# Optimization experiments

Hardware: AMD Instinct MI355X
Metric: run time of the kernel (lower is better)

## Reference

```python
import jax, jax.numpy as jnp
import numpy as np

N, D, DEG, DEPTH, H = 50000, 300, 6, 3, 4
E = N * DEG
DK = D // H


def setup_inputs() -> dict:
    key = jax.random.key(0)
    ks = jax.random.split(key, 14)
    # circulant molecular-like graph: node i <-> i+k (k=1,2,3), edges emitted in
    # reverse pairs (2t, 2t+1) as required by reverse_edge()
    u = np.arange(N)
    src_l, dst_l = [], []
    for k in (1, 2, 3):
        v = (u + k) % N
        src_l.append(np.stack([u, v], 1).reshape(-1))
        dst_l.append(np.stack([v, u], 1).reshape(-1))
    src = np.concatenate(src_l).astype(np.int32)
    dst = np.concatenate(dst_l).astype(np.int32)
    # incoming-edge ids per node (every node has exactly DEG in-edges)
    order = np.argsort(dst, kind='stable')
    nbr_eids = order.reshape(N, DEG).astype(np.int32)
    nbr_mask = np.ones((N, DEG), dtype=bool)
    sd = 1.0 / np.sqrt(D)
    p = lambda i, shape: jax.random.normal(ks[i], shape, jnp.float32) * sd
    return {
        'f': jax.random.normal(ks[0], (N, D), jnp.float32),
        'x': jax.random.normal(ks[1], (E, D), jnp.float32),
        'Wq': p(2, (D, D)), 'bq': jnp.zeros((D,), jnp.float32),
        'Wk': p(3, (D, D)), 'bk': jnp.zeros((D,), jnp.float32),
        'Wv': p(4, (D, D)), 'bv': jnp.zeros((D,), jnp.float32),
        'Wo': p(5, (D, D)), 'bo': jnp.zeros((D,), jnp.float32),
        'W_mp': p(6, (DEPTH - 1, D, D)), 'b_mp': jnp.zeros((DEPTH - 1, D), jnp.float32),
        'W_last': p(7, (3 * D, D)), 'b_last': jnp.zeros((D,), jnp.float32),
        'src': jnp.asarray(src), 'dst': jnp.asarray(dst),
        'nbr_eids': jnp.asarray(nbr_eids), 'nbr_mask': jnp.asarray(nbr_mask),
    }


def reference(f, x, Wq, bq, Wk, bk, Wv, bv, Wo, bo, W_mp, b_mp, W_last, b_last,
              src, dst, nbr_eids, nbr_mask):
    n = f.shape[0]
    e = x.shape[0]
    rev = jnp.arange(e) ^ 1                     # reverse-pair permutation
    has_in = nbr_mask.any(axis=-1)              # [N]
    scale = 1.0 / jnp.sqrt(jnp.float32(DK))
    h = x                                       # edge state 'h' init from 'x'
    f_h = f                                     # node state 'f_h' init from 'f'
    for i in range(DEPTH - 1):
        # ragged mailbox of incoming edge states, padded to DEG
        m = jnp.where(nbr_mask[..., None], h[nbr_eids], 0.0)        # [N,DEG,D]
        q = (f_h @ Wq + bq).reshape(n, H, DK)                        # query = node feat
        k = (m @ Wk + bk).reshape(n, DEG, H, DK)                     # key   = mailbox
        v = ((m + f_h[:, None, :]) @ Wv + bv).reshape(n, DEG, H, DK) # value = mailbox + feat
        scores = jnp.einsum('nhk,ndhk->nhd', q, k) * scale          # [N,H,DEG]
        scores = jnp.where(nbr_mask[:, None, :], scores, -1e9)
        attn = jax.nn.softmax(scores, axis=-1)
        out = jnp.einsum('nhd,ndhk->nhk', attn, v).reshape(n, D) @ Wo + bo
        f_h = jnp.where(has_in[:, None], out, f_h)
        # edge update: m = f_h[src] - rev_h; h = relu(x + Linear_i(m))
        m_e = f_h[src] - h[rev]
        h = jax.nn.relu(x + m_e @ W_mp[i] + b_mp[i])
    # GEANet is undefined in the provided source -> identity pass-through
    mail = jax.ops.segment_sum(h, dst, num_segments=n)              # sum of in-edge states
    f_new = jnp.concatenate([mail, f_h, f], axis=-1) @ W_last + b_last
    f_final = jnp.where(has_in[:, None], f_new, f_h)
    return f_final, h
```

## Files before the change

kernel.cpp:

```cpp
#include <hip/hip_runtime.h>
#include <hip/hip_bf16.h>

typedef unsigned long long ull;
typedef unsigned int u32;
typedef unsigned short u16;
typedef __hip_bfloat16 bf16;
typedef __attribute__((ext_vector_type(8))) short v8s;
typedef __attribute__((ext_vector_type(4))) float v4f;
typedef __attribute__((ext_vector_type(2))) ull v2u;

#define NN 50000
#define DD 300
#define PD 320
#define EE (NN*6)

__device__ __forceinline__ u16 f2bf(float f) {
    u32 u = __float_as_uint(f);
    u32 r = u + 0x7FFFu + ((u >> 16) & 1u);
    return (u16)(r >> 16);
}
__device__ __forceinline__ float bf2f(u16 b) { return __uint_as_float(((u32)b) << 16); }

__device__ __forceinline__ ull sub4bf(ull a, ull b) {
    ull r = 0;
    #pragma unroll
    for (int i = 0; i < 4; ++i) {
        float fa = bf2f((u16)(a >> (16 * i)));
        float fb = bf2f((u16)(b >> (16 * i)));
        r |= ((ull)f2bf(fa - fb)) << (16 * i);
    }
    return r;
}

enum { A_DIR = 0, A_MPG = 1, A_CAT = 2 };
enum { E_BIAS = 0, E_RELUX = 1 };
enum { O_F32 = 1, O_BF16 = 2, O_BOTH = 3 };

template<int AMODE, int EPI, int OUTM, int NW, int NSEG>
__global__ __launch_bounds__(NW*64)
void gemm_mfma(const bf16* __restrict__ A0, const bf16* __restrict__ A1,
               const bf16* __restrict__ A2, const bf16* __restrict__ A3,
               const bf16* __restrict__ A4,
               const int* __restrict__ srcidx, const bf16* __restrict__ BT,
               const float* __restrict__ bias0, const float* __restrict__ bias1,
               const bf16* __restrict__ xepi,
               float* __restrict__ Cf, bf16* __restrict__ Cb0, bf16* __restrict__ Cb1,
               int M)
{
    __shared__ __align__(16) char Als[64 * 640];
    const int tid = threadIdx.x;
    const int wave = tid >> 6, lane = tid & 63;
    const int l15 = lane & 15, l4 = lane >> 4;
    const int wv = (NW == 8) ? (wave & 3) : wave;
    const int half = (NW == 8) ? (wave >> 2) : 0;
    const int rowBase = blockIdx.x * 64;
    const int T = NW * 64;

    v4f acc[4][5];
    const v4f vzero = {0.f, 0.f, 0.f, 0.f};
    #pragma unroll
    for (int mt = 0; mt < 4; ++mt)
        #pragma unroll
        for (int nt = 0; nt < 5; ++nt) acc[mt][nt] = vzero;

    for (int seg = 0; seg < NSEG; ++seg) {
        const bf16* As = (seg == 0) ? A0 : (seg == 1 ? A1 : (seg == 2 ? A2 :
                         (seg == 3 ? A3 : A4)));
        if (seg) __syncthreads();
        #pragma unroll
        for (int s = 0; s < 2560 / T; ++s) {
            int c = tid + T * s;
            int r = c / 40, ch = c - r * 40;
            int grow = rowBase + r;
            int gc = (grow < M) ? grow : 0;
            v2u v;
            if (AMODE == A_MPG) {
                int s0 = srcidx[gc];
                v2u a = *(const v2u*)(A0 + (long)s0 * PD + ch * 8);
                v2u b = *(const v2u*)(A1 + (long)(gc ^ 1) * PD + ch * 8);
                v[0] = sub4bf(a[0], b[0]);
                v[1] = sub4bf(a[1], b[1]);
            } else {
                v = *(const v2u*)(As + (long)gc * PD + ch * 8);
            }
            *(v2u*)(Als + ((c * 16) ^ ((r & 7) << 4))) = v;
        }
        __syncthreads();

        const bf16* BTs = BT + (long)seg * 320 * PD;
        #pragma unroll
        for (int ks = 0; ks < 10; ++ks) {
            v8s af[4];
            #pragma unroll
            for (int mt = 0; mt < 4; ++mt) {
                int rowL = mt * 16 + l15;
                af[mt] = *(const v8s*)(Als +
                    ((rowL * 640 + ks * 64 + l4 * 16) ^ ((rowL & 7) << 4)));
            }
            #pragma unroll
            for (int nt = 0; nt < 5; ++nt) {
                int col = wave * 80 + nt * 16 + l15;
                v8s bfr = *(const v8s*)(BTs + (long)col * PD + ks * 32 + l4 * 8);
                #pragma unroll
                for (int mt = 0; mt < 4; ++mt)
                    acc[mt][nt] = __builtin_amdgcn_mfma_f32_16x16x32_bf16(
                        af[mt], bfr, acc[mt][nt], 0, 0, 0);
            }
        }
        if (seg + 1 < NSEG) __syncthreads();
    }

    const int NOUT = (NW == 8) ? 2 : 1;
    #pragma unroll
    for (int oh = 0; oh < NOUT; ++oh) {
        __syncthreads();
        if (half == oh) {
            const float* bias = oh ? bias1 : bias0;
            #pragma unroll
            for (int nt = 0; nt < 5; ++nt) {
                int col = wv * 80 + nt * 16 + l15;
                float bvv = bias ? bias[col] : 0.f;
                #pragma unroll
                for (int mt = 0; mt < 4; ++mt) {
                    #pragma unroll
                    for (int r = 0; r < 4; ++r) {
                        int rowL = mt * 16 + l4 * 4 + r;
                        *(u16*)(Als + ((rowL * 640 + col * 2) ^ (((rowL >> 2) & 7) << 4)))
                            = f2bf(acc[mt][nt][r] + bvv);
                    }
                }
            }
        }
        __syncthreads();
        {
            bf16* Cb = oh ? Cb1 : Cb0;
            #pragma unroll
            for (int s = 0; s < 2560 / T; ++s) {
                int c = tid + T * s;
                int r = c / 40, ch = c - r * 40;
                int grow = rowBase + r;
                if (grow >= M) continue;
                v2u val = *(const v2u*)(Als + ((c * 16) ^ (((r >> 2) & 7) << 4)));
                if (EPI == E_RELUX) {
                    v2u xv = *(const v2u*)(xepi + (long)grow * PD + ch * 8);
                    #pragma unroll
                    for (int w = 0; w < 2; ++w) {
                        ull rr = 0;
                        #pragma unroll
                        for (int i = 0; i < 4; ++i) {
                            float fv = bf2f((u16)(val[w] >> (16 * i))) +
                                       bf2f((u16)(xv[w] >> (16 * i)));
                            fv = fmaxf(fv, 0.f);
                            rr |= ((ull)f2bf(fv)) << (16 * i);
                        }
                        val[w] = rr;
                    }
                }
                if (OUTM & O_BF16)
                    *(v2u*)(Cb + (long)grow * PD + ch * 8) = val;
                if (OUTM & O_F32) {
                    int col0 = ch * 8;
                    if (col0 < DD) {
                        float4 lo;
                        lo.x = bf2f((u16)(val[0]));
                        lo.y = bf2f((u16)(val[0] >> 16));
                        lo.z = bf2f((u16)(val[0] >> 32));
                        lo.w = bf2f((u16)(val[0] >> 48));
                        *(float4*)(Cf + (long)grow * DD + col0) = lo;
                        if (col0 + 4 < DD) {
                            float4 hi;
                            hi.x = bf2f((u16)(val[1]));
                            hi.y = bf2f((u16)(val[1] >> 16));
                            hi.z = bf2f((u16)(val[1] >> 32));
                            hi.w = bf2f((u16)(val[1] >> 48));
                            *(float4*)(Cf + (long)grow * DD + col0 + 4) = hi;
                        }
                    }
                }
            }
        }
    }
}

__global__ __launch_bounds__(256)
void scoreU_k(const bf16* __restrict__ G0, const bf16* __restrict__ G1,
              const bf16* __restrict__ G2, const bf16* __restrict__ G3,
              const bf16* __restrict__ h, const int* __restrict__ nbr,
              bf16* __restrict__ U0, bf16* __restrict__ U1,
              bf16* __restrict__ U2, bf16* __restrict__ U3)
{
    int wave = threadIdx.x >> 6, lane = threadIdx.x & 63;
    int n = blockIdx.x * 4 + wave;
    if (n >= NN) return;
    int eid[6];
    #pragma unroll
    for (int d = 0; d < 6; ++d) eid[d] = nbr[n * 6 + d];

    bool act = lane < 40;
    int cl = act ? lane : 0;
    long go = (long)n * PD + cl * 8;

    float g[4][8];
    #pragma unroll
    for (int hh = 0; hh < 4; ++hh) {
        const bf16* Gp = (hh == 0) ? G0 : (hh == 1) ? G1 : (hh == 2) ? G2 : G3;
        v2u gv = *(const v2u*)(Gp + go);
        #pragma unroll
        for (int i = 0; i < 8; ++i)
            g[hh][i] = act ? bf2f((u16)(gv[i >> 2] >> ((i & 3) * 16))) : 0.f;
    }
    v2u hp[6];
    #pragma unroll
    for (int d = 0; d < 6; ++d)
        hp[d] = *(const v2u*)(h + (long)eid[d] * PD + cl * 8);

    float s0[6], s1[6], s2[6], s3[6];
    #pragma unroll
    for (int d = 0; d < 6; ++d) {
        float p0 = 0, p1 = 0, p2 = 0, p3 = 0;
        #pragma unroll
        for (int i = 0; i < 8; ++i) {
            float hf = bf2f((u16)(hp[d][i >> 2] >> ((i & 3) * 16)));
            p0 += g[0][i] * hf;
            p1 += g[1][i] * hf;
            p2 += g[2][i] * hf;
            p3 += g[3][i] * hf;
        }
        #pragma unroll
        for (int off = 32; off; off >>= 1) {
            p0 += __shfl_xor(p0, off);
            p1 += __shfl_xor(p1, off);
            p2 += __shfl_xor(p2, off);
            p3 += __shfl_xor(p3, off);
        }
        s0[d] = p0; s1[d] = p1; s2[d] = p2; s3[d] = p3;
    }

    const float scale = 0.1154700538379252f;
    float at[4][6];
    {
        float m0 = -1e30f, m1 = -1e30f, m2 = -1e30f, m3 = -1e30f;
        #pragma unroll
        for (int d = 0; d < 6; ++d) {
            s0[d] *= scale; s1[d] *= scale; s2[d] *= scale; s3[d] *= scale;
            m0 = fmaxf(m0, s0[d]); m1 = fmaxf(m1, s1[d]);
            m2 = fmaxf(m2, s2[d]); m3 = fmaxf(m3, s3[d]);
        }
        float t0 = 0, t1 = 0, t2 = 0, t3 = 0;
        #pragma unroll
        for (int d = 0; d < 6; ++d) {
            at[0][d] = expf(s0[d] - m0); t0 += at[0][d];
            at[1][d] = expf(s1[d] - m1); t1 += at[1][d];
            at[2][d] = expf(s2[d] - m2); t2 += at[2][d];
            at[3][d] = expf(s3[d] - m3); t3 += at[3][d];
        }
        t0 = 1.f / t0; t1 = 1.f / t1; t2 = 1.f / t2; t3 = 1.f / t3;
        #pragma unroll
        for (int d = 0; d < 6; ++d) {
            at[0][d] *= t0; at[1][d] *= t1; at[2][d] *= t2; at[3][d] *= t3;
        }
    }

    float u[4][8];
    #pragma unroll
    for (int hh = 0; hh < 4; ++hh)
        #pragma unroll
        for (int i = 0; i < 8; ++i) u[hh][i] = 0.f;
    #pragma unroll
    for (int d = 0; d < 6; ++d) {
        #pragma unroll
        for (int i = 0; i < 8; ++i) {
            float hf = bf2f((u16)(hp[d][i >> 2] >> ((i & 3) * 16)));
            u[0][i] += at[0][d] * hf;
            u[1][i] += at[1][d] * hf;
            u[2][i] += at[2][d] * hf;
            u[3][i] += at[3][d] * hf;
        }
    }
    if (act) {
        #pragma unroll
        for (int hh = 0; hh < 4; ++hh) {
            bf16* Up = (hh == 0) ? U0 : (hh == 1) ? U1 : (hh == 2) ? U2 : U3;
            v2u r;
            r[0] = (ull)f2bf(u[hh][0]) | ((ull)f2bf(u[hh][1]) << 16) |
                   ((ull)f2bf(u[hh][2]) << 32) | ((ull)f2bf(u[hh][3]) << 48);
            r[1] = (ull)f2bf(u[hh][4]) | ((ull)f2bf(u[hh][5]) << 16) |
                   ((ull)f2bf(u[hh][6]) << 32) | ((ull)f2bf(u[hh][7]) << 48);
            *(v2u*)(Up + go) = r;
        }
    }
}

__global__ __launch_bounds__(256)
void mail_k(const bf16* __restrict__ h, const int* __restrict__ nbr,
            bf16* __restrict__ mail)
{
    int idx = blockIdx.x * 256 + threadIdx.x;
    if (idx >= NN * 40) return;
    int n = idx / 40, ch = idx - n * 40;
    const int* e = nbr + n * 6;
    float s[8] = {0, 0, 0, 0, 0, 0, 0, 0};
    #pragma unroll
    for (int d = 0; d < 6; ++d) {
        v2u v = *(const v2u*)(h + (long)e[d] * PD + ch * 8);
        #pragma unroll
        for (int i = 0; i < 8; ++i)
            s[i] += bf2f((u16)(v[i >> 2] >> ((i & 3) * 16)));
    }
    v2u r;
    r[0] = (ull)f2bf(s[0]) | ((ull)f2bf(s[1]) << 16) |
           ((ull)f2bf(s[2]) << 32) | ((ull)f2bf(s[3]) << 48);
    r[1] = (ull)f2bf(s[4]) | ((ull)f2bf(s[5]) << 16) |
           ((ull)f2bf(s[6]) << 32) | ((ull)f2bf(s[7]) << 48);
    *(v2u*)(mail + (long)n * PD + ch * 8) = r;
}

__global__ __launch_bounds__(256)
void conv_k(const float* __restrict__ in, bf16* __restrict__ out, int rows)
{
    long idx = (long)blockIdx.x * 256 + threadIdx.x;
    if (idx >= (long)rows * 40) return;
    int r = (int)(idx / 40), ch = (int)(idx - (long)r * 40);
    int c4 = ch * 2;
    float4 a = {0, 0, 0, 0}, b = {0, 0, 0, 0};
    if (c4 < 75)     a = *(const float4*)(in + (long)r * DD + c4 * 4);
    if (c4 + 1 < 75) b = *(const float4*)(in + (long)r * DD + c4 * 4 + 4);
    v2u v;
    v[0] = (ull)f2bf(a.x) | ((ull)f2bf(a.y) << 16) |
           ((ull)f2bf(a.z) << 32) | ((ull)f2bf(a.w) << 48);
    v[1] = (ull)f2bf(b.x) | ((ull)f2bf(b.y) << 16) |
           ((ull)f2bf(b.z) << 32) | ((ull)f2bf(b.w) << 48);
    *(v2u*)(out + (long)r * PD + ch * 8) = v;
}

__global__ __launch_bounds__(256)
void tw_k(const float* __restrict__ W, bf16* __restrict__ BT)
{
    int idx = blockIdx.x * 256 + threadIdx.x;
    if (idx >= 320 * 320) return;
    int nn = idx / 320, kk = idx - nn * 320;
    u16 v = 0;
    if (nn < DD && kk < DD) v = f2bf(W[kk * DD + nn]);
    ((u16*)BT)[idx] = v;
}

__global__ __launch_bounds__(256)
void wqk_k(const float* __restrict__ Wq, const float* __restrict__ Wk,
           bf16* __restrict__ slab, int hbase)
{
    int idx = blockIdx.x * 256 + threadIdx.x;
    if (idx >= 640 * 320) return;
    int c = idx / 320, k = idx - c * 320;
    int hh = hbase + (c >= 320 ? 1 : 0);
    int ci = (c >= 320) ? (c - 320) : c;
    float v = 0.f;
    if (ci < DD && k < DD) {
        int jb = hh * 75;
        for (int j = 0; j < 75; ++j)
            v += Wq[k * DD + jb + j] * Wk[ci * DD + jb + j];
    }
    ((u16*)slab)[idx] = f2bf(v);
}

__global__ __launch_bounds__(256)
void wcomp_k(const float* __restrict__ Wv, const float* __restrict__ Wo,
             bf16* __restrict__ slab)
{
    int idx = blockIdx.x * 256 + threadIdx.x;
    if (idx >= 5 * 320 * 320) return;
    int s = idx / 102400, rem = idx - s * 102400;
    int c = rem / 320, k = rem - c * 320;
    float v = 0.f;
    if (c < DD && k < DD) {
        int jb = (s < 4) ? s * 75 : 0;
        int jn = (s < 4) ? 75 : 300;
        for (int j = 0; j < jn; ++j)
            v += Wv[k * DD + jb + j] * Wo[(jb + j) * DD + c];
    }
    ((u16*)slab)[idx] = f2bf(v);
}

__global__ void bias_k(const float* __restrict__ Wk, const float* __restrict__ Wo,
                       const float* __restrict__ bq, const float* __restrict__ bv,
                       const float* __restrict__ bo, const float* __restrict__ bmp,
                       const float* __restrict__ blast, float* __restrict__ outb)
{
    int a = blockIdx.x, i = threadIdx.x;
    float v = 0.f;
    if (i < DD) {
        if (a < 4) {
            for (int j = 0; j < 75; ++j) v += bq[a * 75 + j] * Wk[i * DD + a * 75 + j];
        } else if (a == 4) {
            for (int j = 0; j < DD; ++j) v += bv[j] * Wo[j * DD + i];
            v += bo[i];
        } else if (a == 5) v = bmp[i];
        else if (a == 6) v = bmp[DD + i];
        else v = blast[i];
    }
    outb[a * 320 + i] = v;
}

extern "C" void kernel_launch(void* const* d_in, const int* in_sizes, int n_in,
                              void* d_out, int out_size, void* d_ws, size_t ws_size,
                              hipStream_t stream)
{
    const float* f     = (const float*)d_in[0];
    const float* x     = (const float*)d_in[1];
    const float* Wq    = (const float*)d_in[2];
    const float* bq    = (const float*)d_in[3];
    const float* Wk    = (const float*)d_in[4];
    const float* bv    = (const float*)d_in[7];
    const float* Wv    = (const float*)d_in[6];
    const float* Wo    = (const float*)d_in[8];
    const float* bo    = (const float*)d_in[9];
    const float* Wmp   = (const float*)d_in[10];
    const float* bmp   = (const float*)d_in[11];
    const float* Wlast = (const float*)d_in[12];
    const float* blast = (const float*)d_in[13];
    const int*   src   = (const int*)d_in[14];
    const int*   nbr   = (const int*)d_in[16];

    float* out     = (float*)d_out;
    float* f_final = out;
    float* h_final = out + (long)NN * DD;

    char* ws = (char*)d_ws;
    bf16* xb  = (bf16*)(ws);
    bf16* h1b = (bf16*)(ws + 192000000LL);
    bf16* h2b = (bf16*)(ws + 384000000LL);
    bf16* fb  = (bf16*)(ws + 576000000LL);
    bf16* G0  = (bf16*)(ws + 608000000LL);
    bf16* G1  = (bf16*)(ws + 640000000LL);
    bf16* G2  = (bf16*)(ws + 672000000LL);
    bf16* G3  = (bf16*)(ws + 704000000LL);
    bf16* FHb = (bf16*)(ws + 736000000LL);
    bf16* WT  = (bf16*)(ws + 768000000LL);
    float* BIAS = (float*)(ws + 772000000LL);
    auto slot = [&](int i) { return WT + (long)i * 320 * 320; };
    bf16* qk01 = slot(0);
    bf16* qk23 = slot(2);
    bf16* fh5  = slot(4);
    bf16* mp0  = slot(9);
    bf16* mp1  = slot(10);
    bf16* lst  = slot(11);
    float* g0p = BIAS;          float* g1p = BIAS + 320;
    float* g2p = BIAS + 640;    float* g3p = BIAS + 960;
    float* b2p = BIAS + 1280;
    float* bm0p = BIAS + 1600;  float* bm1p = BIAS + 1920;
    float* blp = BIAS + 2240;
    bf16* MLb = G0;

    dim3 blk(256), blk8(512);
    const int gE = (EE + 63) / 64;
    const int gN = (NN + 63) / 64;

    conv_k<<<(int)(((long)EE * 40 + 255) / 256), blk, 0, stream>>>(x, xb, EE);
    conv_k<<<(int)(((long)NN * 40 + 255) / 256), blk, 0, stream>>>(f, fb, NN);
    wqk_k<<<800, blk, 0, stream>>>(Wq, Wk, qk01, 0);
    wqk_k<<<800, blk, 0, stream>>>(Wq, Wk, qk23, 2);
    wcomp_k<<<2000, blk, 0, stream>>>(Wv, Wo, fh5);
    tw_k<<<400, blk, 0, stream>>>(Wmp, mp0);
    tw_k<<<400, blk, 0, stream>>>(Wmp + 90000, mp1);
    tw_k<<<400, blk, 0, stream>>>(Wlast, lst);
    tw_k<<<400, blk, 0, stream>>>(Wlast + 90000, slot(12));
    tw_k<<<400, blk, 0, stream>>>(Wlast + 180000, slot(13));
    bias_k<<<8, 320, 0, stream>>>(Wk, Wo, bq, bv, bo, bmp, blast, BIAS);

    for (int it = 0; it < 2; ++it) {
        const bf16* hb  = it ? h1b : xb;
        const bf16* fhb = it ? FHb : fb;
        gemm_mfma<A_DIR, E_BIAS, O_BF16, 8, 1><<<gN, blk8, 0, stream>>>(
            fhb, nullptr, nullptr, nullptr, nullptr, nullptr, qk01,
            g0p, g1p, nullptr, nullptr, G0, G1, NN);
        gemm_mfma<A_DIR, E_BIAS, O_BF16, 8, 1><<<gN, blk8, 0, stream>>>(
            fhb, nullptr, nullptr, nullptr, nullptr, nullptr, qk23,
            g2p, g3p, nullptr, nullptr, G2, G3, NN);
        scoreU_k<<<(NN + 3) / 4, blk, 0, stream>>>(G0, G1, G2, G3, hb, nbr,
                                                   G0, G1, G2, G3);
        gemm_mfma<A_CAT, E_BIAS, O_BF16, 4, 5><<<gN, blk, 0, stream>>>(
            G0, G1, G2, G3, fhb, nullptr, fh5, b2p, nullptr, nullptr,
            nullptr, FHb, nullptr, NN);
        if (it == 0) {
            gemm_mfma<A_MPG, E_RELUX, O_BF16, 4, 1><<<gE, blk, 0, stream>>>(
                FHb, hb, nullptr, nullptr, nullptr, src, mp0, bm0p, nullptr,
                xb, nullptr, h1b, nullptr, EE);
        } else {
            gemm_mfma<A_MPG, E_RELUX, O_BOTH, 4, 1><<<gE, blk, 0, stream>>>(
                FHb, hb, nullptr, nullptr, nullptr, src, mp1, bm1p, nullptr,
                xb, h_final, h2b, nullptr, EE);
        }
    }

    mail_k<<<(NN * 40 + 255) / 256, blk, 0, stream>>>(h2b, nbr, MLb);
    gemm_mfma<A_CAT, E_BIAS, O_F32, 4, 3><<<gN, blk, 0, stream>>>(
        MLb, FHb, fb, nullptr, nullptr, nullptr, lst, blp, nullptr, nullptr,
        f_final, nullptr, nullptr, NN);
}
```

Before: 2.311 ms.

## Use packed bf16 conversion, merge QK GEMMs, drop bf16 h copy, transpose weights

Replaces per-element bf16 rounding and unpacking with the v_cvt_pk_bf16_f32 instruction and mask/shift unpacking. The two Q·K projection GEMM launches become one launch with a 2-wide grid.y that offsets weights, biases and outputs per slice. The final edge-update GEMM now writes only the fp32 output, and the mailbox sum reads that fp32 h directly, removing the separate bf16 h buffer write. Weight preprocessing transposes Wq/Wk/Wv first so the precompute kernels read coalesced. The mailbox kernel now reads twice the bytes per edge in fp32, trading that against the dropped bf16 store.

```diff
diff --git a/kernel.cpp b/kernel.cpp
--- a/kernel.cpp
+++ b/kernel.cpp
@@ -19,17 +19,21 @@
     u32 r = u + 0x7FFFu + ((u >> 16) & 1u);
     return (u16)(r >> 16);
 }
-__device__ __forceinline__ float bf2f(u16 b) { return __uint_as_float(((u32)b) << 16); }
-
+__device__ __forceinline__ u32 cvtpk(float lo, float hi) {
+    u32 r;
+    asm("v_cvt_pk_bf16_f32 %0, %1, %2" : "=v"(r) : "v"(lo), "v"(hi));
+    return r;
+}
+__device__ __forceinline__ float lo16(u32 u) { return __uint_as_float(u << 16); }
+__device__ __forceinline__ float hi16(u32 u) { return __uint_as_float(u & 0xffff0000u); }
+
+__device__ __forceinline__ u32 sub2bf(u32 a, u32 b) {
+    return cvtpk(lo16(a) - lo16(b), hi16(a) - hi16(b));
+}
 __device__ __forceinline__ ull sub4bf(ull a, ull b) {
-    ull r = 0;
-    #pragma unroll
-    for (int i = 0; i < 4; ++i) {
-        float fa = bf2f((u16)(a >> (16 * i)));
-        float fb = bf2f((u16)(b >> (16 * i)));
-        r |= ((ull)f2bf(fa - fb)) << (16 * i);
-    }
-    return r;
+    u32 l = sub2bf((u32)a, (u32)b);
+    u32 h = sub2bf((u32)(a >> 32), (u32)(b >> 32));
+    return (ull)l | ((ull)h << 32);
 }
 
 enum { A_DIR = 0, A_MPG = 1, A_CAT = 2 };
@@ -45,7 +49,7 @@
                const float* __restrict__ bias0, const float* __restrict__ bias1,
                const bf16* __restrict__ xepi,
                float* __restrict__ Cf, bf16* __restrict__ Cb0, bf16* __restrict__ Cb1,
-               int M)
+               int M, int ybias, long ycb)
 {
     __shared__ __align__(16) char Als[64 * 640];
     const int tid = threadIdx.x;
@@ -55,6 +59,12 @@
     const int half = (NW == 8) ? (wave >> 2) : 0;
     const int rowBase = blockIdx.x * 64;
     const int T = NW * 64;
+    const int gy = blockIdx.y;
+    BT += (long)gy * 204800;
+    if (bias0) bias0 += (long)gy * ybias;
+    if (bias1) bias1 += (long)gy * ybias;
+    if (Cb0) Cb0 += gy * ycb;
+    if (Cb1) Cb1 += gy * ycb;
 
     v4f acc[4][5];
     const v4f vzero = {0.f, 0.f, 0.f, 0.f};
@@ -145,15 +155,13 @@
                     v2u xv = *(const v2u*)(xepi + (long)grow * PD + ch * 8);
                     #pragma unroll
                     for (int w = 0; w < 2; ++w) {
-                        ull rr = 0;
-                        #pragma unroll
-                        for (int i = 0; i < 4; ++i) {
-                            float fv = bf2f((u16)(val[w] >> (16 * i))) +
-                                       bf2f((u16)(xv[w] >> (16 * i)));
-                            fv = fmaxf(fv, 0.f);
-                            rr |= ((ull)f2bf(fv)) << (16 * i);
-                        }
-                        val[w] = rr;
+                        u32 a0 = (u32)val[w], a1 = (u32)(val[w] >> 32);
+                        u32 x0 = (u32)xv[w],  x1 = (u32)(xv[w] >> 32);
+                        u32 r0 = cvtpk(fmaxf(lo16(a0) + lo16(x0), 0.f),
+                                       fmaxf(hi16(a0) + hi16(x0), 0.f));
+                        u32 r1 = cvtpk(fmaxf(lo16(a1) + lo16(x1), 0.f),
+                                       fmaxf(hi16(a1) + hi16(x1), 0.f));
+                        val[w] = (ull)r0 | ((ull)r1 << 32);
                     }
                 }
                 if (OUTM & O_BF16)
@@ -161,18 +169,12 @@
                 if (OUTM & O_F32) {
                     int col0 = ch * 8;
                     if (col0 < DD) {
-                        float4 lo;
-                        lo.x = bf2f((u16)(val[0]));
-                        lo.y = bf2f((u16)(val[0] >> 16));
-                        lo.z = bf2f((u16)(val[0] >> 32));
-                        lo.w = bf2f((u16)(val[0] >> 48));
+                        u32 a0 = (u32)val[0], a1 = (u32)(val[0] >> 32);
+                        float4 lo = {lo16(a0), hi16(a0), lo16(a1), hi16(a1)};
                         *(float4*)(Cf + (long)grow * DD + col0) = lo;
                         if (col0 + 4 < DD) {
-                            float4 hi;
-                            hi.x = bf2f((u16)(val[1]));
-                            hi.y = bf2f((u16)(val[1] >> 16));
-                            hi.z = bf2f((u16)(val[1] >> 32));
-                            hi.w = bf2f((u16)(val[1] >> 48));
+                            u32 b0 = (u32)val[1], b1 = (u32)(val[1] >> 32);
+                            float4 hi = {lo16(b0), hi16(b0), lo16(b1), hi16(b1)};
                             *(float4*)(Cf + (long)grow * DD + col0 + 4) = hi;
                         }
                     }
@@ -205,9 +207,15 @@
     for (int hh = 0; hh < 4; ++hh) {
         const bf16* Gp = (hh == 0) ? G0 : (hh == 1) ? G1 : (hh == 2) ? G2 : G3;
         v2u gv = *(const v2u*)(Gp + go);
-        #pragma unroll
-        for (int i = 0; i < 8; ++i)
-            g[hh][i] = act ? bf2f((u16)(gv[i >> 2] >> ((i & 3) * 16))) : 0.f;
+        u32 w0 = (u32)gv[0], w1 = (u32)(gv[0] >> 32);
+        u32 w2 = (u32)gv[1], w3 = (u32)(gv[1] >> 32);
+        g[hh][0] = lo16(w0); g[hh][1] = hi16(w0);
+        g[hh][2] = lo16(w1); g[hh][3] = hi16(w1);
+        g[hh][4] = lo16(w2); g[hh][5] = hi16(w2);
+        g[hh][6] = lo16(w3); g[hh][7] = hi16(w3);
+        if (!act)
+            #pragma unroll
+            for (int i = 0; i < 8; ++i) g[hh][i] = 0.f;
     }
     v2u hp[6];
     #pragma unroll
@@ -217,14 +225,17 @@
     float s0[6], s1[6], s2[6], s3[6];
     #pragma unroll
     for (int d = 0; d < 6; ++d) {
+        u32 w0 = (u32)hp[d][0], w1 = (u32)(hp[d][0] >> 32);
+        u32 w2 = (u32)hp[d][1], w3 = (u32)(hp[d][1] >> 32);
+        float hf[8] = {lo16(w0), hi16(w0), lo16(w1), hi16(w1),
+                       lo16(w2), hi16(w2), lo16(w3), hi16(w3)};
         float p0 = 0, p1 = 0, p2 = 0, p3 = 0;
         #pragma unroll
         for (int i = 0; i < 8; ++i) {
-            float hf = bf2f((u16)(hp[d][i >> 2] >> ((i & 3) * 16)));
-            p0 += g[0][i] * hf;
-            p1 += g[1][i] * hf;
-            p2 += g[2][i] * hf;
-            p3 += g[3][i] * hf;
+            p0 += g[0][i] * hf[i];
+            p1 += g[1][i] * hf[i];
+            p2 += g[2][i] * hf[i];
+            p3 += g[3][i] * hf[i];
         }
         #pragma unroll
         for (int off = 32; off; off >>= 1) {
@@ -268,13 +279,16 @@
         for (int i = 0; i < 8; ++i) u[hh][i] = 0.f;
     #pragma unroll
     for (int d = 0; d < 6; ++d) {
+        u32 w0 = (u32)hp[d][0], w1 = (u32)(hp[d][0] >> 32);
+        u32 w2 = (u32)hp[d][1], w3 = (u32)(hp[d][1] >> 32);
+        float hf[8] = {lo16(w0), hi16(w0), lo16(w1), hi16(w1),
+                       lo16(w2), hi16(w2), lo16(w3), hi16(w3)};
         #pragma unroll
         for (int i = 0; i < 8; ++i) {
-            float hf = bf2f((u16)(hp[d][i >> 2] >> ((i & 3) * 16)));
-            u[0][i] += at[0][d] * hf;
-            u[1][i] += at[1][d] * hf;
-            u[2][i] += at[2][d] * hf;
-            u[3][i] += at[3][d] * hf;
+            u[0][i] += at[0][d] * hf[i];
+            u[1][i] += at[1][d] * hf[i];
+            u[2][i] += at[2][d] * hf[i];
+            u[3][i] += at[3][d] * hf[i];
         }
     }
     if (act) {
@@ -282,37 +296,33 @@
         for (int hh = 0; hh < 4; ++hh) {
             bf16* Up = (hh == 0) ? U0 : (hh == 1) ? U1 : (hh == 2) ? U2 : U3;
             v2u r;
-            r[0] = (ull)f2bf(u[hh][0]) | ((ull)f2bf(u[hh][1]) << 16) |
-                   ((ull)f2bf(u[hh][2]) << 32) | ((ull)f2bf(u[hh][3]) << 48);
-            r[1] = (ull)f2bf(u[hh][4]) | ((ull)f2bf(u[hh][5]) << 16) |
-                   ((ull)f2bf(u[hh][6]) << 32) | ((ull)f2bf(u[hh][7]) << 48);
+            r[0] = (ull)cvtpk(u[hh][0], u[hh][1]) |
+                   ((ull)cvtpk(u[hh][2], u[hh][3]) << 32);
+            r[1] = (ull)cvtpk(u[hh][4], u[hh][5]) |
+                   ((ull)cvtpk(u[hh][6], u[hh][7]) << 32);
             *(v2u*)(Up + go) = r;
         }
     }
 }
 
 __global__ __launch_bounds__(256)
-void mail_k(const bf16* __restrict__ h, const int* __restrict__ nbr,
-            bf16* __restrict__ mail)
+void mailf_k(const float* __restrict__ h, const int* __restrict__ nbr,
+             bf16* __restrict__ mail)
 {
     int idx = blockIdx.x * 256 + threadIdx.x;
-    if (idx >= NN * 40) return;
-    int n = idx / 40, ch = idx - n * 40;
-    const int* e = nbr + n * 6;
-    float s[8] = {0, 0, 0, 0, 0, 0, 0, 0};
-    #pragma unroll
-    for (int d = 0; d < 6; ++d) {
-        v2u v = *(const v2u*)(h + (long)e[d] * PD + ch * 8);
-        #pragma unroll
-        for (int i = 0; i < 8; ++i)
-            s[i] += bf2f((u16)(v[i >> 2] >> ((i & 3) * 16)));
-    }
-    v2u r;
-    r[0] = (ull)f2bf(s[0]) | ((ull)f2bf(s[1]) << 16) |
-           ((ull)f2bf(s[2]) << 32) | ((ull)f2bf(s[3]) << 48);
-    r[1] = (ull)f2bf(s[4]) | ((ull)f2bf(s[5]) << 16) |
-           ((ull)f2bf(s[6]) << 32) | ((ull)f2bf(s[7]) << 48);
-    *(v2u*)(mail + (long)n * PD + ch * 8) = r;
+    if (idx >= NN * 80) return;
+    int n = idx / 80, c4 = idx - n * 80;
+    float4 s = {0.f, 0.f, 0.f, 0.f};
+    if (c4 < 75) {
+        const int* e = nbr + n * 6;
+        #pragma unroll
+        for (int d = 0; d < 6; ++d) {
+            float4 v = *(const float4*)(h + (long)e[d] * DD + c4 * 4);
+            s.x += v.x; s.y += v.y; s.z += v.z; s.w += v.w;
+        }
+    }
+    ull r = (ull)cvtpk(s.x, s.y) | ((ull)cvtpk(s.z, s.w) << 32);
+    *(ull*)(mail + (long)n * PD + c4 * 4) = r;
 }
 
 __global__ __launch_bounds__(256)
@@ -326,10 +336,8 @@
     if (c4 < 75)     a = *(const float4*)(in + (long)r * DD + c4 * 4);
     if (c4 + 1 < 75) b = *(const float4*)(in + (long)r * DD + c4 * 4 + 4);
     v2u v;
-    v[0] = (ull)f2bf(a.x) | ((ull)f2bf(a.y) << 16) |
-           ((ull)f2bf(a.z) << 32) | ((ull)f2bf(a.w) << 48);
-    v[1] = (ull)f2bf(b.x) | ((ull)f2bf(b.y) << 16) |
-           ((ull)f2bf(b.z) << 32) | ((ull)f2bf(b.w) << 48);
+    v[0] = (ull)cvtpk(a.x, a.y) | ((ull)cvtpk(a.z, a.w) << 32);
+    v[1] = (ull)cvtpk(b.x, b.y) | ((ull)cvtpk(b.z, b.w) << 32);
     *(v2u*)(out + (long)r * PD + ch * 8) = v;
 }
 
@@ -345,25 +353,43 @@
 }
 
 __global__ __launch_bounds__(256)
-void wqk_k(const float* __restrict__ Wq, const float* __restrict__ Wk,
-           bf16* __restrict__ slab, int hbase)
+void twf_k(const float* __restrict__ W, float* __restrict__ WT)
+{
+    __shared__ float t[32][33];
+    int bx = blockIdx.x % 10, by = blockIdx.x / 10;
+    int r0 = by * 32, c0 = bx * 32;
+    int tx = threadIdx.x & 31, ty = threadIdx.x >> 5;
+    #pragma unroll
+    for (int i = 0; i < 4; ++i) {
+        int r = r0 + ty + i * 8, c = c0 + tx;
+        t[ty + i * 8][tx] = (r < DD && c < DD) ? W[r * DD + c] : 0.f;
+    }
+    __syncthreads();
+    #pragma unroll
+    for (int i = 0; i < 4; ++i)
+        WT[(c0 + ty + i * 8) * 320 + r0 + tx] = t[tx][ty + i * 8];
+}
+
+__global__ __launch_bounds__(256)
+void wqk_k(const float* __restrict__ WqT, const float* __restrict__ Wk,
+           bf16* __restrict__ slab)
 {
     int idx = blockIdx.x * 256 + threadIdx.x;
-    if (idx >= 640 * 320) return;
+    if (idx >= 1280 * 320) return;
     int c = idx / 320, k = idx - c * 320;
-    int hh = hbase + (c >= 320 ? 1 : 0);
-    int ci = (c >= 320) ? (c - 320) : c;
+    int hh = c / 320;
+    int ci = c - hh * 320;
     float v = 0.f;
     if (ci < DD && k < DD) {
         int jb = hh * 75;
         for (int j = 0; j < 75; ++j)
-            v += Wq[k * DD + jb + j] * Wk[ci * DD + jb + j];
+            v += WqT[(jb + j) * 320 + k] * Wk[ci * DD + jb + j];
     }
     ((u16*)slab)[idx] = f2bf(v);
 }
 
 __global__ __launch_bounds__(256)
-void wcomp_k(const float* __restrict__ Wv, const float* __restrict__ Wo,
+void wcomp_k(const float* __restrict__ WvT, const float* __restrict__ Wo,
              bf16* __restrict__ slab)
 {
     int idx = blockIdx.x * 256 + threadIdx.x;
@@ -375,12 +401,12 @@
         int jb = (s < 4) ? s * 75 : 0;
         int jn = (s < 4) ? 75 : 300;
         for (int j = 0; j < jn; ++j)
-            v += Wv[k * DD + jb + j] * Wo[(jb + j) * DD + c];
+            v += WvT[(jb + j) * 320 + k] * Wo[(jb + j) * DD + c];
     }
     ((u16*)slab)[idx] = f2bf(v);
 }
 
-__global__ void bias_k(const float* __restrict__ Wk, const float* __restrict__ Wo,
+__global__ void bias_k(const float* __restrict__ WkT, const float* __restrict__ Wo,
                        const float* __restrict__ bq, const float* __restrict__ bv,
                        const float* __restrict__ bo, const float* __restrict__ bmp,
                        const float* __restrict__ blast, float* __restrict__ outb)
@@ -389,7 +415,8 @@
     float v = 0.f;
     if (i < DD) {
         if (a < 4) {
-            for (int j = 0; j < 75; ++j) v += bq[a * 75 + j] * Wk[i * DD + a * 75 + j];
+            for (int j = 0; j < 75; ++j)
+                v += bq[a * 75 + j] * WkT[(a * 75 + j) * 320 + i];
         } else if (a == 4) {
             for (int j = 0; j < DD; ++j) v += bv[j] * Wo[j * DD + i];
             v += bo[i];
@@ -427,7 +454,6 @@
     char* ws = (char*)d_ws;
     bf16* xb  = (bf16*)(ws);
     bf16* h1b = (bf16*)(ws + 192000000LL);
-    bf16* h2b = (bf16*)(ws + 384000000LL);
     bf16* fb  = (bf16*)(ws + 576000000LL);
     bf16* G0  = (bf16*)(ws + 608000000LL);
     bf16* G1  = (bf16*)(ws + 640000000LL);
@@ -436,63 +462,63 @@
     bf16* FHb = (bf16*)(ws + 736000000LL);
     bf16* WT  = (bf16*)(ws + 768000000LL);
     float* BIAS = (float*)(ws + 772000000LL);
+    float* WqT  = (float*)(ws + 772100000LL);
+    float* WkT  = (float*)(ws + 772600000LL);
+    float* WvT  = (float*)(ws + 773100000LL);
     auto slot = [&](int i) { return WT + (long)i * 320 * 320; };
-    bf16* qk01 = slot(0);
-    bf16* qk23 = slot(2);
+    bf16* qk   = slot(0);
     bf16* fh5  = slot(4);
     bf16* mp0  = slot(9);
     bf16* mp1  = slot(10);
     bf16* lst  = slot(11);
     float* g0p = BIAS;          float* g1p = BIAS + 320;
-    float* g2p = BIAS + 640;    float* g3p = BIAS + 960;
     float* b2p = BIAS + 1280;
     float* bm0p = BIAS + 1600;  float* bm1p = BIAS + 1920;
     float* blp = BIAS + 2240;
     bf16* MLb = G0;
 
     dim3 blk(256), blk8(512);
+    const int gN = (NN + 63) / 64;
     const int gE = (EE + 63) / 64;
-    const int gN = (NN + 63) / 64;
 
     conv_k<<<(int)(((long)EE * 40 + 255) / 256), blk, 0, stream>>>(x, xb, EE);
     conv_k<<<(int)(((long)NN * 40 + 255) / 256), blk, 0, stream>>>(f, fb, NN);
-    wqk_k<<<800, blk, 0, stream>>>(Wq, Wk, qk01, 0);
-    wqk_k<<<800, blk, 0, stream>>>(Wq, Wk, qk23, 2);
-    wcomp_k<<<2000, blk, 0, stream>>>(Wv, Wo, fh5);
+    twf_k<<<100, blk, 0, stream>>>(Wq, WqT);
+    twf_k<<<100, blk, 0, stream>>>(Wk, WkT);
+    twf_k<<<100, blk, 0, stream>>>(Wv, WvT);
+    wqk_k<<<1600, blk, 0, stream>>>(WqT, Wk, qk);
+    wcomp_k<<<2000, blk, 0, stream>>>(WvT, Wo, fh5);
     tw_k<<<400, blk, 0, stream>>>(Wmp, mp0);
     tw_k<<<400, blk, 0, stream>>>(Wmp + 90000, mp1);
     tw_k<<<400, blk, 0, stream>>>(Wlast, lst);
     tw_k<<<400, blk, 0, stream>>>(Wlast + 90000, slot(12));
     tw_k<<<400, blk, 0, stream>>>(Wlast + 180000, slot(13));
-    bias_k<<<8, 320, 0, stream>>>(Wk, Wo, bq, bv, bo, bmp, blast, BIAS);
+    bias_k<<<8, 320, 0, stream>>>(WkT, Wo, bq, bv, bo, bmp, blast, BIAS);
 
     for (int it = 0; it < 2; ++it) {
         const bf16* hb  = it ? h1b : xb;
         const bf16* fhb = it ? FHb : fb;
-        gemm_mfma<A_DIR, E_BIAS, O_BF16, 8, 1><<<gN, blk8, 0, stream>>>(
-            fhb, nullptr, nullptr, nullptr, nullptr, nullptr, qk01,
-            g0p, g1p, nullptr, nullptr, G0, G1, NN);
-        gemm_mfma<A_DIR, E_BIAS, O_BF16, 8, 1><<<gN, blk8, 0, stream>>>(
-            fhb, nullptr, nullptr, nullptr, nullptr, nullptr, qk23,
-            g2p, g3p, nullptr, nullptr, G2, G3, NN);
+        gemm_mfma<A_DIR, E_BIAS, O_BF16, 8, 1><<<dim3(gN, 2), blk8, 0, stream>>>(
+            fhb, nullptr, nullptr, nullptr, nullptr, nullptr, qk,
+            g0p, g1p, nullptr, nullptr, G0, G1, NN, 640, 32000000);
         scoreU_k<<<(NN + 3) / 4, blk, 0, stream>>>(G0, G1, G2, G3, hb, nbr,
                                                    G0, G1, G2, G3);
         gemm_mfma<A_CAT, E_BIAS, O_BF16, 4, 5><<<gN, blk, 0, stream>>>(
             G0, G1, G2, G3, fhb, nullptr, fh5, b2p, nullptr, nullptr,
-            nullptr, FHb, nullptr, NN);
+            nullptr, FHb, nullptr, NN, 0, 0);
         if (it == 0) {
             gemm_mfma<A_MPG, E_RELUX, O_BF16, 4, 1><<<gE, blk, 0, stream>>>(
                 FHb, hb, nullptr, nullptr, nullptr, src, mp0, bm0p, nullptr,
-                xb, nullptr, h1b, nullptr, EE);
+                xb, nullptr, h1b, nullptr, EE, 0, 0);
         } else {
-            gemm_mfma<A_MPG, E_RELUX, O_BOTH, 4, 1><<<gE, blk, 0, stream>>>(
+            gemm_mfma<A_MPG, E_RELUX, O_F32, 4, 1><<<gE, blk, 0, stream>>>(
                 FHb, hb, nullptr, nullptr, nullptr, src, mp1, bm1p, nullptr,
-                xb, h_final, h2b, nullptr, EE);
-        }
-    }
-
-    mail_k<<<(NN * 40 + 255) / 256, blk, 0, stream>>>(h2b, nbr, MLb);
+                xb, h_final, nullptr, nullptr, EE, 0, 0);
+        }
+    }
+
+    mailf_k<<<(NN * 80 + 255) / 256, blk, 0, stream>>>(h_final, nbr, MLb);
     gemm_mfma<A_CAT, E_BIAS, O_F32, 4, 3><<<gN, blk, 0, stream>>>(
         MLb, FHb, fb, nullptr, nullptr, nullptr, lst, blp, nullptr, nullptr,
-        f_final, nullptr, nullptr, NN);
-}
+        f_final, nullptr, nullptr, NN, 0, 0);
+}
```

New measurement: 2.151 ms. -6.9%, faster.
